# Optimization experiments

Hardware: AMD Instinct MI355X
Metric: run time of the kernel (lower is better)

Reference implementation:

```python
import jax, jax.numpy as jnp
import numpy as np

V, E = 50000, 400000
ND, ED, OUT = 128, 64, 128  # node feat, edge feat, out_dim
IN = ND + ED
NEG_SLOPE = 0.01
BN_EPS = 1e-5


def setup_inputs() -> dict:
    key = jax.random.key(0)
    ks = jax.random.split(key, 12)
    s = lambda d: 1.0 / np.sqrt(d)
    return {
        "node_feats": jax.random.normal(ks[0], (V, ND), jnp.float32),
        "edge_feats": jax.random.normal(ks[1], (E, ED), jnp.float32),
        "src": jax.random.randint(ks[2], (E,), 0, V, jnp.int32),
        "dst": jax.random.randint(ks[3], (E,), 0, V, jnp.int32),
        "W1": jax.random.uniform(ks[4], (IN, OUT), jnp.float32, -s(IN), s(IN)),
        "b1": jnp.zeros((OUT,), jnp.float32),
        "W2": jax.random.uniform(ks[5], (OUT, OUT), jnp.float32, -s(OUT), s(OUT)),
        "b2": jnp.zeros((OUT,), jnp.float32),
        "W3": jax.random.uniform(ks[6], (OUT, OUT), jnp.float32, -s(OUT), s(OUT)),
        "b3": jnp.zeros((OUT,), jnp.float32),
        "gamma": jnp.ones((OUT,), jnp.float32),
        "beta": jnp.zeros((OUT,), jnp.float32),
    }


def _lrelu(x):
    return jnp.where(x >= 0, x, NEG_SLOPE * x)


def reference(node_feats, edge_feats, src, dst, W1, b1, W2, b2, W3, b3, gamma, beta):
    # u_add_v: gather source + destination node features per edge  [E, ND]
    m = node_feats[src] + node_feats[dst]
    # concat edge feats with message: [E, ED+ND] = [E, IN]
    x = jnp.concatenate([edge_feats, m], axis=1)
    h = _lrelu(x @ W1 + b1)
    h = _lrelu(h @ W2 + b2)
    h = _lrelu(h @ W3 + b3)
    # dropout p=0 -> identity; BatchNorm1d (training mode, batch stats over edges)
    mean = jnp.mean(h, axis=0)
    var = jnp.mean((h - mean) ** 2, axis=0)  # biased variance
    return gamma * (h - mean) * jax.lax.rsqrt(var + BN_EPS) + beta
```

## Files before the change

kernel.cpp:

```cpp
#include <hip/hip_runtime.h>
#include <hip/hip_bf16.h>
#include <cstddef>

#define N_E 400000
#define N_V 50000
#define NEG_SLOPE 0.01f
#define BN_EPS 1e-5f
#define NT (N_E / 64)

typedef __attribute__((ext_vector_type(8))) short bf16x8;
typedef __attribute__((ext_vector_type(4))) short s16x4;
typedef __attribute__((ext_vector_type(4))) float f32x4;

#define PART_OFF   0
#define SCALE_OFF  65536
#define WT_OFF     66560
#define META_END   181248
#define Y_BYTES    12800000ULL
#define H_BYTES    102400000ULL
#define OUT_BYTES  204800000ULL

#define SWX(row, chunk) ((row) * 64 + ((((chunk) ^ ((row) & 7))) << 3))
#define SWM(row, chunk) ((row) * 128 + ((((chunk) ^ ((row) & 7))) << 3))

__device__ __forceinline__ unsigned short f2bf(float f) {
  unsigned u = __builtin_bit_cast(unsigned, f);
  u += 0x7fffu + ((u >> 16) & 1u);
  return (unsigned short)(u >> 16);
}
__device__ __forceinline__ float bf2f(unsigned short s) {
  return __builtin_bit_cast(float, (unsigned)s << 16);
}
__device__ __forceinline__ float lrelu(float x) {
  return x >= 0.f ? x : NEG_SLOPE * x;
}
__device__ __forceinline__ unsigned pk2(float lo, float hi) {
  unsigned r;
  asm("v_cvt_pk_bf16_f32 %0, %1, %2" : "=v"(r) : "v"(lo), "v"(hi));
  return r;
}
__device__ __forceinline__ int addbf(int a, int b) {
  unsigned ua = (unsigned)a, ub = (unsigned)b;
  float l = __builtin_bit_cast(float, ua << 16) + __builtin_bit_cast(float, ub << 16);
  float h = __builtin_bit_cast(float, ua & 0xffff0000u) +
            __builtin_bit_cast(float, ub & 0xffff0000u);
  return (int)pk2(l, h);
}

template<bool USEWS>
__global__ __launch_bounds__(512, 8) void gnn8(
    const float* __restrict__ edgef, const int* __restrict__ srcI,
    const int* __restrict__ dstI, const short* __restrict__ ybuf,
    const float* __restrict__ b1, const float* __restrict__ b2,
    const float* __restrict__ b3, const short* __restrict__ wt,
    float* __restrict__ partials, short* __restrict__ hout,
    float* __restrict__ fout) {
  __shared__ short sX[64 * 64];
  __shared__ short sY[64 * 128];
  __shared__ short sZ[64 * 128];

  const int tid = threadIdx.x;
  const int lane = tid & 63;
  const int w = tid >> 6;
  const int col = lane & 15;
  const int lq = lane >> 4;
  const int t = blockIdx.x;
  const int r8 = tid >> 3, c8 = tid & 7;
  const int f0 = w * 16 + lq * 4;
  const int ch = f0 >> 3, sub = f0 & 7;

  {
    int e = t * 64 + r8;
    int si = srcI[e], di = dstI[e];
    const float4* efp = (const float4*)(edgef + (size_t)e * 64) + c8 * 2;
    float4 e0 = efp[0], e1 = efp[1];
    const int4* yps = (const int4*)(ybuf + (size_t)si * 128) + c8 * 2;
    const int4* ypd = (const int4*)(ybuf + (size_t)di * 128) + c8 * 2;
    int4 a0 = yps[0], a1 = yps[1];
    int4 d0 = ypd[0], d1 = ypd[1];
    int4 x;
    x.x = (int)pk2(e0.x, e0.y); x.y = (int)pk2(e0.z, e0.w);
    x.z = (int)pk2(e1.x, e1.y); x.w = (int)pk2(e1.z, e1.w);
    *(int4*)(sX + SWX(r8, c8)) = x;
    int4 y0, y1;
    y0.x = addbf(a0.x, d0.x); y0.y = addbf(a0.y, d0.y);
    y0.z = addbf(a0.z, d0.z); y0.w = addbf(a0.w, d0.w);
    y1.x = addbf(a1.x, d1.x); y1.y = addbf(a1.y, d1.y);
    y1.z = addbf(a1.z, d1.z); y1.w = addbf(a1.w, d1.w);
    *(int4*)(sY + SWM(r8, c8 * 2)) = y0;
    *(int4*)(sY + SWM(r8, c8 * 2 + 1)) = y1;
  }

  f32x4 acc[4];
  #pragma unroll
  for (int i = 0; i < 4; ++i) acc[i] = (f32x4){0.f, 0.f, 0.f, 0.f};
  float sE[4] = {0.f, 0.f, 0.f, 0.f}, sQv[4] = {0.f, 0.f, 0.f, 0.f};

  __syncthreads();

  {
    #pragma unroll
    for (int s = 0; s < 2; ++s) {
      bf16x8 f1 = *(const bf16x8*)(wt + (((w * 2 + s) << 9) + lane * 8));
      #pragma unroll
      for (int et = 0; et < 4; ++et) {
        bf16x8 b = *(const bf16x8*)(sX + SWX(et * 16 + col, lq + s * 4));
        acc[et] = __builtin_amdgcn_mfma_f32_16x16x32_bf16(f1, b, acc[et], 0, 0, 0);
      }
    }
    float4 bb = *(const float4*)(b1 + f0);
    #pragma unroll
    for (int et = 0; et < 4; ++et) {
      const int edge = et * 16 + col;
      short4 q = *(const short4*)(sY + SWM(edge, ch) + sub);
      f32x4 a = acc[et];
      float v0 = lrelu(a[0] + bb.x + bf2f((unsigned short)q.x));
      float v1 = lrelu(a[1] + bb.y + bf2f((unsigned short)q.y));
      float v2 = lrelu(a[2] + bb.z + bf2f((unsigned short)q.z));
      float v3 = lrelu(a[3] + bb.w + bf2f((unsigned short)q.w));
      *(int2*)(sZ + SWM(edge, ch) + sub) = make_int2((int)pk2(v0, v1), (int)pk2(v2, v3));
      acc[et] = (f32x4){0.f, 0.f, 0.f, 0.f};
    }
  }
  __syncthreads();

  {
    #pragma unroll
    for (int s = 0; s < 4; ++s) {
      bf16x8 f2 = *(const bf16x8*)(wt + 24576 + (((w * 4 + s) << 9) + lane * 8));
      #pragma unroll
      for (int et = 0; et < 4; ++et) {
        bf16x8 b = *(const bf16x8*)(sZ + SWM(et * 16 + col, lq + s * 4));
        acc[et] = __builtin_amdgcn_mfma_f32_16x16x32_bf16(f2, b, acc[et], 0, 0, 0);
      }
    }
    float4 bb = *(const float4*)(b2 + f0);
    #pragma unroll
    for (int et = 0; et < 4; ++et) {
      const int edge = et * 16 + col;
      f32x4 a = acc[et];
      float v0 = lrelu(a[0] + bb.x), v1 = lrelu(a[1] + bb.y);
      float v2 = lrelu(a[2] + bb.z), v3 = lrelu(a[3] + bb.w);
      *(int2*)(sY + SWM(edge, ch) + sub) = make_int2((int)pk2(v0, v1), (int)pk2(v2, v3));
      acc[et] = (f32x4){0.f, 0.f, 0.f, 0.f};
    }
  }
  __syncthreads();

  {
    #pragma unroll
    for (int s = 0; s < 4; ++s) {
      bf16x8 f3 = *(const bf16x8*)(wt + 40960 + (((w * 4 + s) << 9) + lane * 8));
      #pragma unroll
      for (int et = 0; et < 4; ++et) {
        bf16x8 b = *(const bf16x8*)(sY + SWM(et * 16 + col, lq + s * 4));
        acc[et] = __builtin_amdgcn_mfma_f32_16x16x32_bf16(f3, b, acc[et], 0, 0, 0);
      }
    }
    float4 bb = *(const float4*)(b3 + f0);
    #pragma unroll
    for (int et = 0; et < 4; ++et) {
      const int edge = et * 16 + col;
      f32x4 a = acc[et];
      float v0 = lrelu(a[0] + bb.x), v1 = lrelu(a[1] + bb.y);
      float v2 = lrelu(a[2] + bb.z), v3 = lrelu(a[3] + bb.w);
      sE[0] += v0; sQv[0] += v0 * v0;
      sE[1] += v1; sQv[1] += v1 * v1;
      sE[2] += v2; sQv[2] += v2 * v2;
      sE[3] += v3; sQv[3] += v3 * v3;
      *(int2*)(sZ + SWM(edge, ch) + sub) = make_int2((int)pk2(v0, v1), (int)pk2(v2, v3));
    }
  }
  __syncthreads();

  if (USEWS) {
    int4* dst = (int4*)(hout + (size_t)t * 8192);
    dst[r8 * 16 + c8 * 2] = *(const int4*)(sZ + SWM(r8, c8 * 2));
    dst[r8 * 16 + c8 * 2 + 1] = *(const int4*)(sZ + SWM(r8, c8 * 2 + 1));
  } else {
    float4* dst = (float4*)(fout + (size_t)t * 8192);
    #pragma unroll
    for (int j = 0; j < 2; ++j) {
      int4 tv = *(const int4*)(sZ + SWM(r8, c8 * 2 + j));
      float4 o0, o1;
      o0.x = bf2f((unsigned short)((unsigned)tv.x & 0xffffu));
      o0.y = bf2f((unsigned short)((unsigned)tv.x >> 16));
      o0.z = bf2f((unsigned short)((unsigned)tv.y & 0xffffu));
      o0.w = bf2f((unsigned short)((unsigned)tv.y >> 16));
      o1.x = bf2f((unsigned short)((unsigned)tv.z & 0xffffu));
      o1.y = bf2f((unsigned short)((unsigned)tv.z >> 16));
      o1.z = bf2f((unsigned short)((unsigned)tv.w & 0xffffu));
      o1.w = bf2f((unsigned short)((unsigned)tv.w >> 16));
      dst[r8 * 32 + c8 * 4 + j * 2] = o0;
      dst[r8 * 32 + c8 * 4 + j * 2 + 1] = o1;
    }
  }

  #pragma unroll
  for (int m = 1; m <= 8; m <<= 1) {
    #pragma unroll
    for (int i = 0; i < 4; ++i) {
      sE[i] += __shfl_xor(sE[i], m, 64);
      sQv[i] += __shfl_xor(sQv[i], m, 64);
    }
  }
  if (col == 0) {
    float* pp = partials + (t & 63) * 256;
    #pragma unroll
    for (int i = 0; i < 4; ++i) {
      atomicAdd(&pp[f0 + i], sE[i]);
      atomicAdd(&pp[128 + f0 + i], sQv[i]);
    }
  }
}

__global__ __launch_bounds__(256) void nodeK(const float* __restrict__ nodef,
                                             const short* __restrict__ wt,
                                             short* __restrict__ y) {
  __shared__ short sN[64 * 136];
  const int tid = threadIdx.x;
  const int lane = tid & 63;
  const int w = tid >> 6;
  const int n0 = blockIdx.x * 64;
  const int r = tid >> 2, p4 = tid & 3;
  {
    int v = n0 + r;
    int vc = v < N_V ? v : N_V - 1;
    const float4* np = (const float4*)(nodef + (size_t)vc * 128) + p4 * 8;
    #pragma unroll
    for (int j = 0; j < 8; ++j) {
      float4 a = np[j];
      *(int2*)(sN + r * 136 + p4 * 32 + j * 4) =
          make_int2((int)pk2(a.x, a.y), (int)pk2(a.z, a.w));
    }
  }
  __syncthreads();
  const short* wb = wt + 8192;
  f32x4 acc[8];
  #pragma unroll
  for (int i = 0; i < 8; ++i) acc[i] = (f32x4){0.f, 0.f, 0.f, 0.f};
  const int col = lane & 15;
  const int kb = (lane >> 4) * 8;
  #pragma unroll
  for (int nt = 0; nt < 2; ++nt)
    #pragma unroll
    for (int s = 0; s < 4; ++s) {
      bf16x8 fr = *(const bf16x8*)(wb + ((((w * 2 + nt) * 4 + s) << 9) + lane * 8));
      #pragma unroll
      for (int et = 0; et < 4; ++et) {
        bf16x8 b = *(const bf16x8*)(sN + (et * 16 + col) * 136 + kb + s * 32);
        acc[nt * 4 + et] = __builtin_amdgcn_mfma_f32_16x16x32_bf16(fr, b, acc[nt * 4 + et], 0, 0, 0);
      }
    }
  __syncthreads();
  {
    const int fb = (lane >> 4) * 4;
    #pragma unroll
    for (int nt = 0; nt < 2; ++nt) {
      const int f0 = w * 32 + nt * 16 + fb;
      #pragma unroll
      for (int et = 0; et < 4; ++et) {
        f32x4 a = acc[nt * 4 + et];
        *(int2*)(sN + (et * 16 + col) * 136 + f0) =
            make_int2((int)pk2(a[0], a[1]), (int)pk2(a[2], a[3]));
      }
    }
  }
  __syncthreads();
  if (n0 + r < N_V) {
    #pragma unroll
    for (int j = 0; j < 4; ++j) {
      int4 tv = *(const int4*)(sN + r * 136 + p4 * 32 + j * 8);
      *(int4*)(y + (size_t)(n0 + r) * 128 + p4 * 32 + j * 8) = tv;
    }
  }
}

__global__ __launch_bounds__(256) void prepK(const float* __restrict__ W1,
                                             const float* __restrict__ W2,
                                             const float* __restrict__ W3,
                                             short* __restrict__ wt,
                                             float* __restrict__ partials) {
  int b = blockIdx.x, t = threadIdx.x;
  if (b < 64) { partials[b * 256 + t] = 0.f; return; }
  int g = (b - 64) * 256 + t;
  for (int fi = g; fi < 57344; fi += 32 * 256) {
    float val;
    if (fi < 8192) {
      int c = fi >> 9, r = fi & 511;
      int l = r >> 3, j = r & 7;
      int tt = c >> 1, s = c & 1;
      int n = tt * 16 + (l & 15);
      int k = s * 32 + (l >> 4) * 8 + j;
      val = W1[k * 128 + n];
    } else if (fi < 24576) {
      int f2 = fi - 8192;
      int c = f2 >> 9, r = f2 & 511;
      int l = r >> 3, j = r & 7;
      int tt = c >> 2, s = c & 3;
      int n = tt * 16 + (l & 15);
      int k = s * 32 + (l >> 4) * 8 + j;
      val = W1[(64 + k) * 128 + n];
    } else if (fi < 40960) {
      int f2 = fi - 24576;
      int c = f2 >> 9, r = f2 & 511;
      int l = r >> 3, j = r & 7;
      int tt = c >> 2, s = c & 3;
      int n = tt * 16 + (l & 15);
      int k = s * 32 + (l >> 4) * 8 + j;
      val = W2[k * 128 + n];
    } else {
      int f3 = fi - 40960;
      int c = f3 >> 9, r = f3 & 511;
      int l = r >> 3, j = r & 7;
      int tt = c >> 2, s = c & 3;
      int n = tt * 16 + (l & 15);
      int k = s * 32 + (l >> 4) * 8 + j;
      val = W3[k * 128 + n];
    }
    wt[fi] = (short)f2bf(val);
  }
}

__global__ __launch_bounds__(256) void statsK(const float* __restrict__ partials,
                                              const float* __restrict__ gamma,
                                              const float* __restrict__ beta,
                                              float* __restrict__ scsh) {
  __shared__ float tmp[256];
  int t = threadIdx.x;
  float a = 0.f;
  #pragma unroll 8
  for (int r = 0; r < 64; ++r) a += partials[r * 256 + t];
  tmp[t] = a;
  __syncthreads();
  if (t < 128) {
    float S = tmp[t], S2 = tmp[t + 128];
    float mean = S / (float)N_E;
    float var = S2 / (float)N_E - mean * mean;
    float inv = rsqrtf(var + BN_EPS);
    float sc = gamma[t] * inv;
    scsh[t] = sc;
    scsh[t + 128] = beta[t] - mean * sc;
  }
}

template<bool USEWS>
__global__ __launch_bounds__(256) void applyK(const short* __restrict__ h,
                                              const float* __restrict__ scsh,
                                              float* out) {
  const int TOT4 = N_E * 128 / 4;
  int j0 = blockIdx.x * 256 + threadIdx.x;
  int c4 = j0 & 31;
  float4 sc = *(const float4*)(scsh + c4 * 4);
  float4 sh = *(const float4*)(scsh + 128 + c4 * 4);
  int stride = gridDim.x * 256;
  for (int j = j0; j < TOT4; j += stride) {
    f32x4 v;
    if (USEWS) {
      s16x4 s = __builtin_nontemporal_load((const s16x4*)(h + (size_t)j * 4));
      v[0] = bf2f((unsigned short)s[0]) * sc.x + sh.x;
      v[1] = bf2f((unsigned short)s[1]) * sc.y + sh.y;
      v[2] = bf2f((unsigned short)s[2]) * sc.z + sh.z;
      v[3] = bf2f((unsigned short)s[3]) * sc.w + sh.w;
    } else {
      f32x4 hv = *((const f32x4*)out + j);
      v[0] = hv[0] * sc.x + sh.x;
      v[1] = hv[1] * sc.y + sh.y;
      v[2] = hv[2] * sc.z + sh.z;
      v[3] = hv[3] * sc.w + sh.w;
    }
    __builtin_nontemporal_store(v, (f32x4*)out + j);
  }
}

extern "C" void kernel_launch(void* const* d_in, const int* in_sizes, int n_in,
                              void* d_out, int out_size, void* d_ws, size_t ws_size,
                              hipStream_t stream) {
  const float* nodef = (const float*)d_in[0];
  const float* edgef = (const float*)d_in[1];
  const int* srcI = (const int*)d_in[2];
  const int* dstI = (const int*)d_in[3];
  const float* W1 = (const float*)d_in[4];
  const float* b1 = (const float*)d_in[5];
  const float* W2 = (const float*)d_in[6];
  const float* b2 = (const float*)d_in[7];
  const float* W3 = (const float*)d_in[8];
  const float* b3 = (const float*)d_in[9];
  const float* gamma = (const float*)d_in[10];
  const float* beta = (const float*)d_in[11];
  float* out = (float*)d_out;
  char* ws = (char*)d_ws;

  float* partials = (float*)(ws + PART_OFF);
  float* scsh = (float*)(ws + SCALE_OFF);
  short* wt = (short*)(ws + WT_OFF);
  short* ybuf;
  short* h = nullptr;
  bool usews;
  if (ws_size >= (size_t)META_END + Y_BYTES + H_BYTES) {
    ybuf = (short*)(ws + META_END);
    h = (short*)(ws + META_END + Y_BYTES);
    usews = true;
  } else if (ws_size >= (size_t)META_END + H_BYTES) {
    h = (short*)(ws + META_END);
    ybuf = (short*)((char*)d_out + OUT_BYTES - Y_BYTES);
    usews = true;
  } else {
    ybuf = (short*)(ws + META_END);
    usews = false;
  }

  prepK<<<96, 256, 0, stream>>>(W1, W2, W3, wt, partials);
  nodeK<<<782, 256, 0, stream>>>(nodef, wt, ybuf);
  if (usews) {
    gnn8<true><<<NT, 512, 0, stream>>>(edgef, srcI, dstI, ybuf, b1, b2, b3,
                                       wt, partials, h, out);
  } else {
    gnn8<false><<<NT, 512, 0, stream>>>(edgef, srcI, dstI, ybuf, b1, b2, b3,
                                        wt, partials, h, out);
  }
  statsK<<<1, 256, 0, stream>>>(partials, gamma, beta, scsh);
  if (usews) {
    applyK<true><<<2048, 256, 0, stream>>>(h, scsh, out);
  } else {
    applyK<false><<<2048, 256, 0, stream>>>(h, scsh, out);
  }
}
```

Baseline: 164.8 us.

## Fuse BN stats into apply kernel and traverse h in reverse for cache reuse

Removes the single-block statsK launch by having every applyK block reduce the 64 partial sums itself and compute scale/shift in shared memory. The apply loop now walks the bf16 h buffer from the end backwards, and uses plain loads instead of nontemporal ones, so the tail that gnn8 just wrote can still be hit in cache. Grid size drops from 2048 to 1024 blocks. The cost is a redundant 64x256 partial reduction in every block.

```diff
diff --git a/kernel.cpp b/kernel.cpp
--- a/kernel.cpp
+++ b/kernel.cpp
@@ -322,54 +322,55 @@
   }
 }
 
-__global__ __launch_bounds__(256) void statsK(const float* __restrict__ partials,
+template<bool USEWS>
+__global__ __launch_bounds__(256) void applyK(const short* __restrict__ h,
+                                              const float* __restrict__ partials,
                                               const float* __restrict__ gamma,
                                               const float* __restrict__ beta,
-                                              float* __restrict__ scsh) {
-  __shared__ float tmp[256];
-  int t = threadIdx.x;
-  float a = 0.f;
-  #pragma unroll 8
-  for (int r = 0; r < 64; ++r) a += partials[r * 256 + t];
-  tmp[t] = a;
+                                              float* out) {
+  __shared__ float sS[256];
+  const int t = threadIdx.x;
+  {
+    float a = 0.f;
+    #pragma unroll 8
+    for (int r = 0; r < 64; ++r) a += partials[r * 256 + t];
+    sS[t] = a;
+  }
   __syncthreads();
   if (t < 128) {
-    float S = tmp[t], S2 = tmp[t + 128];
+    float S = sS[t], S2 = sS[t + 128];
     float mean = S / (float)N_E;
     float var = S2 / (float)N_E - mean * mean;
     float inv = rsqrtf(var + BN_EPS);
     float sc = gamma[t] * inv;
-    scsh[t] = sc;
-    scsh[t + 128] = beta[t] - mean * sc;
-  }
-}
-
-template<bool USEWS>
-__global__ __launch_bounds__(256) void applyK(const short* __restrict__ h,
-                                              const float* __restrict__ scsh,
-                                              float* out) {
+    sS[t] = sc;
+    sS[t + 128] = beta[t] - mean * sc;
+  }
+  __syncthreads();
+
   const int TOT4 = N_E * 128 / 4;
-  int j0 = blockIdx.x * 256 + threadIdx.x;
-  int c4 = j0 & 31;
-  float4 sc = *(const float4*)(scsh + c4 * 4);
-  float4 sh = *(const float4*)(scsh + 128 + c4 * 4);
+  int j0 = blockIdx.x * 256 + t;
+  int c4 = (TOT4 - 1 - j0) & 31;
+  float4 sc = *(const float4*)(sS + c4 * 4);
+  float4 sh = *(const float4*)(sS + 128 + c4 * 4);
   int stride = gridDim.x * 256;
   for (int j = j0; j < TOT4; j += stride) {
+    int jj = TOT4 - 1 - j;
     f32x4 v;
     if (USEWS) {
-      s16x4 s = __builtin_nontemporal_load((const s16x4*)(h + (size_t)j * 4));
+      s16x4 s = *(const s16x4*)(h + (size_t)jj * 4);
       v[0] = bf2f((unsigned short)s[0]) * sc.x + sh.x;
       v[1] = bf2f((unsigned short)s[1]) * sc.y + sh.y;
       v[2] = bf2f((unsigned short)s[2]) * sc.z + sh.z;
       v[3] = bf2f((unsigned short)s[3]) * sc.w + sh.w;
     } else {
-      f32x4 hv = *((const f32x4*)out + j);
+      f32x4 hv = *((const f32x4*)out + jj);
       v[0] = hv[0] * sc.x + sh.x;
       v[1] = hv[1] * sc.y + sh.y;
       v[2] = hv[2] * sc.z + sh.z;
       v[3] = hv[3] * sc.w + sh.w;
     }
-    __builtin_nontemporal_store(v, (f32x4*)out + j);
+    __builtin_nontemporal_store(v, (f32x4*)out + jj);
   }
 }
 
@@ -392,7 +393,6 @@
   char* ws = (char*)d_ws;
 
   float* partials = (float*)(ws + PART_OFF);
-  float* scsh = (float*)(ws + SCALE_OFF);
   short* wt = (short*)(ws + WT_OFF);
   short* ybuf;
   short* h = nullptr;
@@ -415,14 +415,10 @@
   if (usews) {
     gnn8<true><<<NT, 512, 0, stream>>>(edgef, srcI, dstI, ybuf, b1, b2, b3,
                                        wt, partials, h, out);
+    applyK<true><<<1024, 256, 0, stream>>>(h, partials, gamma, beta, out);
   } else {
     gnn8<false><<<NT, 512, 0, stream>>>(edgef, srcI, dstI, ybuf, b1, b2, b3,
                                         wt, partials, h, out);
-  }
-  statsK<<<1, 256, 0, stream>>>(partials, gamma, beta, scsh);
-  if (usews) {
-    applyK<true><<<2048, 256, 0, stream>>>(h, scsh, out);
-  } else {
-    applyK<false><<<2048, 256, 0, stream>>>(h, scsh, out);
-  }
-}
+    applyK<false><<<1024, 256, 0, stream>>>(h, partials, gamma, beta, out);
+  }
+}
```

Measured after the change: 153.8 us, median of 3. 1.07x faster.
